# Optimization experiments

Measured on AMD Instinct MI355X. Metric: run time of the kernel, lower is better.

The kernel has to match this reference:

```python
import jax, jax.numpy as jnp
import numpy as np

B, S, H, D = 2, 2048, 16, 64  # batch, seq, heads, head_dim


def setup_inputs() -> dict:
    key = jax.random.key(0)
    kq, kk, kv = jax.random.split(key, 3)
    query = jax.random.normal(kq, (B, S, H, D), dtype=jnp.float32)
    key_l = jax.random.normal(kk, (B, S, H, D), dtype=jnp.float32)
    value = jax.random.normal(kv, (B, S, H, D), dtype=jnp.float32)
    # padding mask: all tokens valid
    attention_mask = jnp.ones((B, S), dtype=bool)
    # causal lower-triangular mask [1,1,S,S]
    causal_mask = jnp.tril(jnp.ones((S, S), dtype=bool))[None, None, :, :]
    return {"query": query, "key": key_l, "value": value,
            "attention_mask": attention_mask, "causal_mask": causal_mask}


def reference(query, key, value, attention_mask, causal_mask):
    b = query.shape[0]
    # broadcast causal mask to batch: (B,1,S,S)
    cm = jnp.broadcast_to(causal_mask, (b,) + causal_mask.shape[1:])
    # padding mask (B,S) -> (B,1,1,S), combine with causal
    am = attention_mask[:, None, None, :]
    mask = jnp.logical_and(cm, am)
    neg = jnp.finfo(query.dtype).min
    bias = jnp.where(mask, jnp.zeros((), query.dtype), jnp.full((), neg, query.dtype))
    sm_scale = 1.0 / jnp.sqrt(jnp.asarray(query.shape[-1], jnp.float32))
    # scores: (B,H,Sq,Sk)
    scores = jnp.einsum("bqhd,bkhd->bhqk", query, key) * sm_scale + bias
    # attention_softmax_in_fp32 = True
    probs = jax.nn.softmax(scores.astype(jnp.float32), axis=-1).astype(query.dtype)
    ctx = jnp.einsum("bhqk,bkhd->bqhd", probs, value)
    # merge heads -> hidden_size_per_partition
    return ctx.reshape(ctx.shape[0], ctx.shape[1], -1)
```

## Files before the change

### kernel.cpp

```cpp
#include <hip/hip_runtime.h>
#include <hip/hip_bf16.h>


typedef __attribute__((ext_vector_type(8))) short short8;
typedef __attribute__((ext_vector_type(4))) short short4v;
typedef __attribute__((ext_vector_type(4))) float f32x4;

__device__ __forceinline__ unsigned cvtpk(float a, float b) {
    __hip_bfloat162 h = __float22bfloat162_rn(make_float2(a, b));
    union { __hip_bfloat162 h; unsigned u; } c; c.h = h;
    return c.u;
}

__device__ __forceinline__ short8 pack8(float4 a, float4 b) {
    union { short8 s; unsigned u[4]; } w;
    w.u[0] = cvtpk(a.x, a.y); w.u[1] = cvtpk(a.z, a.w);
    w.u[2] = cvtpk(b.x, b.y); w.u[3] = cvtpk(b.z, b.w);
    return w.s;
}

__device__ __forceinline__ unsigned short f2b(float v) {
    union { __hip_bfloat16 h; unsigned short u; } c;
    c.h = __float2bfloat16(v);
    return c.u;
}

__device__ __forceinline__ float b2f(unsigned short u) {
    union { unsigned u; float f; } v; v.u = ((unsigned)u) << 16;
    return v.f;
}

#define TR64(dst, addr) \
    asm volatile("ds_read_b64_tr_b16 %0, %1" : "=v"(dst) : "v"(addr))

#define GLOAD_LDS16(g, l) \
    __builtin_amdgcn_global_load_lds((const __attribute__((address_space(1))) void*)(g), \
                                     (__attribute__((address_space(3))) void*)(l), 16, 0, 0)

__constant__ unsigned char JOBS[24][3] = {
    {15,0,16},{7,0,16},{14,0,15},{14,15,30},{13,14,28},{6,0,14},{12,13,26},{11,12,24},
    {15,16,32},{13,0,14},{12,0,13},{10,0,11},{10,11,22},{9,0,10},{11,0,12},{5,0,12},
    {0,0,2},{1,0,4},{2,0,6},{3,0,8},{8,0,9},{9,10,20},{8,9,18},{4,0,10}
};

__global__ __launch_bounds__(256, 4)
void CoreAttention_68710886801875_prepass(const float* __restrict__ K,
                                          const float* __restrict__ V,
                                          unsigned short* __restrict__ Kbf,
                                          unsigned short* __restrict__ Vbf)
{
    const int tile = blockIdx.x;
    const int bh = tile >> 5, kt = tile & 31;
    const size_t base = (size_t)(bh >> 4) * (2048 * 1024) + (size_t)(bh & 15) * 64;
    unsigned short* ktile = Kbf + (size_t)tile * 4096;
    unsigned short* vtile = Vbf + (size_t)tile * 4096;

#pragma unroll
    for (int it = 0; it < 2; ++it) {
        const int c = threadIdx.x + it * 256;
        {
            const int r  = c >> 3;
            const int c8 = (c & 7) ^ (r & 7);
            const float* src = K + base + (size_t)(kt * 64 + r) * 1024 + c8 * 8;
            *(short8*)(ktile + c * 8) = pack8(*(const float4*)src, *(const float4*)(src + 4));
        }
        {
            const int s = c >> 3, k_lo = (c >> 1) & 3, half = c & 1;
            const int k  = (s >> 2) * 4 + k_lo;
            const int c8 = (s & 3) * 2 + half;
            const float* src = V + base + (size_t)(kt * 64 + k) * 1024 + c8 * 8;
            *(short8*)(vtile + c * 8) = pack8(*(const float4*)src, *(const float4*)(src + 4));
        }
    }
}

template <int PRE>
__global__ __launch_bounds__(256, 3)
void CoreAttention_68710886801875_kernel(const float* __restrict__ Q,
                                         const float* __restrict__ K,
                                         const float* __restrict__ V,
                                         const unsigned short* __restrict__ Kbf,
                                         const unsigned short* __restrict__ Vbf,
                                         float* __restrict__ O,
                                         unsigned short* __restrict__ Opart,
                                         float* __restrict__ Lpart)
{
    constexpr int S = 2048, HD = 1024;
    constexpr float SCALE = 0.125f * 1.44269504088896340736f;

    __shared__ __align__(16) unsigned short ldsK[2][64 * 64];
    __shared__ __align__(16) unsigned short ldsV[2][64 * 64];
    __shared__ __align__(16) unsigned short ldsPT[4][2][64 * 16];

    const int tid = threadIdx.x;
    const int wid = tid >> 6, lane = tid & 63, g = lane >> 4, lm = lane & 15;

    const int bx     = blockIdx.x;
    const int r_     = bx >> 3;
    const int jobIdx = r_ >> 2;
    const int bh     = (bx & 7) * 4 + (r_ & 3);
    const int qt     = JOBS[jobIdx][0];
    const int t0     = JOBS[jobIdx][1];
    const int t1     = JOBS[jobIdx][2];
    const int b      = bh >> 4, h = bh & 15;
    const int q0     = qt << 7;
    const int diagT  = 2 * qt + (wid >> 1);
    const int nd     = (wid & 1) << 1;
    const size_t base = ((size_t)b * S) * HD + (size_t)h * 64;

    const int r0 = tid >> 3, c8 = tid & 7;
    const float* kp0 = K + base + (size_t)r0 * HD + c8 * 8;
    const float* vp0 = V + base + (size_t)r0 * HD + c8 * 8;
    float4 kst[4], vst[4];
    const unsigned short* kbfB = Kbf + (size_t)bh * 32 * 4096;
    const unsigned short* vbfB = Vbf + (size_t)bh * 32 * 4096;

    auto STAGE_ISSUE = [&](int kt2, int buf) {
        if constexpr (PRE) {
            const unsigned short* ks = kbfB + (size_t)kt2 * 4096 + tid * 8;
            const unsigned short* vs = vbfB + (size_t)kt2 * 4096 + tid * 8;
            GLOAD_LDS16(ks,        &ldsK[buf][tid * 8]);
            GLOAD_LDS16(ks + 2048, &ldsK[buf][tid * 8 + 2048]);
            GLOAD_LDS16(vs,        &ldsV[buf][tid * 8]);
            GLOAD_LDS16(vs + 2048, &ldsV[buf][tid * 8 + 2048]);
        } else {
            const float* kp = kp0 + (size_t)kt2 * 64 * HD;
            const float* vp = vp0 + (size_t)kt2 * 64 * HD;
            kst[0] = *(const float4*)kp;
            kst[1] = *(const float4*)(kp + 4);
            kst[2] = *(const float4*)(kp + (size_t)32 * HD);
            kst[3] = *(const float4*)(kp + (size_t)32 * HD + 4);
            vst[0] = *(const float4*)vp;
            vst[1] = *(const float4*)(vp + 4);
            vst[2] = *(const float4*)(vp + (size_t)32 * HD);
            vst[3] = *(const float4*)(vp + (size_t)32 * HD + 4);
        }
    };
    auto STAGE_WRITE = [&](int buf) {
        if constexpr (!PRE) {
#pragma unroll
            for (int it = 0; it < 2; ++it) {
                const int r = r0 + it * 32;
                const unsigned byteK = (unsigned)((r * 128 + c8 * 16) ^ ((r & 7) << 4));
                *(short8*)((char*)&ldsK[buf][0] + byteK) = pack8(kst[it * 2], kst[it * 2 + 1]);
                const unsigned byteV = (unsigned)(((r >> 2) * 4 + (c8 >> 1)) * 128 +
                                                  (r & 3) * 32 + (c8 & 1) * 16);
                *(short8*)((char*)&ldsV[buf][0] + byteV) = pack8(vst[it * 2], vst[it * 2 + 1]);
            }
        }
    };

    short8 qf[2][2];
#pragma unroll
    for (int m = 0; m < 2; ++m) {
        const float* qp = Q + base + (size_t)(q0 + wid * 32 + m * 16 + lm) * HD + g * 8;
#pragma unroll
        for (int ks = 0; ks < 2; ++ks) {
            float4 a = *(const float4*)(qp + ks * 32);
            float4 cc = *(const float4*)(qp + ks * 32 + 4);
            a.x *= SCALE; a.y *= SCALE; a.z *= SCALE; a.w *= SCALE;
            cc.x *= SCALE; cc.y *= SCALE; cc.z *= SCALE; cc.w *= SCALE;
            qf[m][ks] = pack8(a, cc);
        }
    }

    short8 ones;
#pragma unroll
    for (int j = 0; j < 8; ++j) ones[j] = (short)0x3F80;

    f32x4 oacc[2][4], lacc[2];
#pragma unroll
    for (int m = 0; m < 2; ++m) {
        lacc[m] = (f32x4){0.f, 0.f, 0.f, 0.f};
#pragma unroll
        for (int n = 0; n < 4; ++n) oacc[m][n] = (f32x4){0.f, 0.f, 0.f, 0.f};
    }

    const unsigned vBase = (unsigned)(size_t)&ldsV[0][0];
    const unsigned ptAddr = (unsigned)(size_t)&ldsPT[wid][0][0];

    STAGE_ISSUE(t0, 0);
    STAGE_WRITE(0);
    __syncthreads();

    for (int t = t0; t < t1; ++t) {
        const int cur = (t - t0) & 1;
        if (t + 1 < t1) STAGE_ISSUE(t + 1, cur ^ 1);

        if (t <= diagT) {
            const bool full = (t < diagT);

            f32x4 sv[2][4];
            __builtin_amdgcn_s_setprio(1);
#pragma unroll
            for (int n = 0; n < 4; ++n) {
                short8 kf0, kf1;
                if (full || n <= nd + 1) {
                    const int kr = n * 16 + lm;
                    const unsigned b0 = cur * 8192u +
                        (unsigned)((kr * 128 + g * 16) ^ ((kr & 7) << 4));
                    const unsigned b1 = cur * 8192u +
                        (unsigned)((kr * 128 + 64 + g * 16) ^ ((kr & 7) << 4));
                    kf0 = *(const short8*)((const char*)&ldsK[0][0] + b0);
                    kf1 = *(const short8*)((const char*)&ldsK[0][0] + b1);
                }
#pragma unroll
                for (int m = 0; m < 2; ++m) {
                    if (full || n <= nd + m) {
                        f32x4 acc = (f32x4){0.f, 0.f, 0.f, 0.f};
                        acc = __builtin_amdgcn_mfma_f32_16x16x32_bf16(qf[m][0], kf0, acc, 0, 0, 0);
                        acc = __builtin_amdgcn_mfma_f32_16x16x32_bf16(qf[m][1], kf1, acc, 0, 0, 0);
                        if (!full && n == nd + m) {
#pragma unroll
                            for (int r = 0; r < 4; ++r)
                                if (lm > g * 4 + r) acc[r] = -1e30f;
                        }
                        sv[m][n] = acc;
                    } else {
                        sv[m][n] = (f32x4){-1e30f, -1e30f, -1e30f, -1e30f};
                    }
                }
            }
            __builtin_amdgcn_s_setprio(0);

#pragma unroll
            for (int m = 0; m < 2; ++m)
#pragma unroll
                for (int n = 0; n < 4; ++n) {
                    float p[4];
#pragma unroll
                    for (int r = 0; r < 4; ++r) p[r] = exp2f(sv[m][n][r]);
                    union { short4v s; unsigned uu[2]; } pk;
                    pk.uu[0] = cvtpk(p[0], p[1]);
                    pk.uu[1] = cvtpk(p[2], p[3]);
                    const unsigned byte = (unsigned)((n * 4 + (lm >> 2)) * 128 +
                                                     (lm & 3) * 32 + g * 8);
                    *(short4v*)((char*)&ldsPT[wid][m][0] + byte) = pk.s;
                }

            asm volatile("s_waitcnt lgkmcnt(0)" ::: "memory");
            short4v vlo[2][4], vhi[2][4], pL[2][2], pH[2][2];
#pragma unroll
            for (int ks = 0; ks < 2; ++ks) {
                const unsigned sub = (unsigned)(8 * ks + 2 * g);
#pragma unroll
                for (int n = 0; n < 4; ++n) {
                    const unsigned va = vBase + cur * 8192u + (sub * 4 + n) * 128 + lm * 8;
                    TR64(vlo[ks][n], va);
                    TR64(vhi[ks][n], va + 512);
                }
#pragma unroll
                for (int m = 0; m < 2; ++m) {
                    const unsigned pa = ptAddr + m * 2048u + sub * 128 + lm * 8;
                    TR64(pL[m][ks], pa);
                    TR64(pH[m][ks], pa + 128);
                }
            }
            asm volatile("s_waitcnt lgkmcnt(0)" ::: "memory");
            __builtin_amdgcn_sched_barrier(0);
            __builtin_amdgcn_s_setprio(1);
#pragma unroll
            for (int m = 0; m < 2; ++m)
#pragma unroll
                for (int ks = 0; ks < 2; ++ks) {
                    const short8 pf = __builtin_shufflevector(pL[m][ks], pH[m][ks],
                                                              0, 1, 2, 3, 4, 5, 6, 7);
                    lacc[m] = __builtin_amdgcn_mfma_f32_16x16x32_bf16(pf, ones, lacc[m], 0, 0, 0);
#pragma unroll
                    for (int n = 0; n < 4; ++n) {
                        const short8 vf = __builtin_shufflevector(vlo[ks][n], vhi[ks][n],
                                                                  0, 1, 2, 3, 4, 5, 6, 7);
                        oacc[m][n] = __builtin_amdgcn_mfma_f32_16x16x32_bf16(pf, vf,
                                                                             oacc[m][n], 0, 0, 0);
                    }
                }
            __builtin_amdgcn_s_setprio(0);
        }

        if (t + 1 < t1) STAGE_WRITE(cur ^ 1);
        __syncthreads();
    }

    if (qt >= 8) {
        const int part = ((bh * 8 + (qt - 8)) << 1) + (t0 != 0 ? 1 : 0);
        unsigned short* op = Opart + (size_t)part * 8192;
        float* lp = Lpart + part * 128;
#pragma unroll
        for (int m = 0; m < 2; ++m)
#pragma unroll
            for (int r = 0; r < 4; ++r) {
                const int row = wid * 32 + m * 16 + g * 4 + r;
                if (lm == 0) lp[row] = lacc[m][r];
#pragma unroll
                for (int n = 0; n < 4; ++n)
                    op[row * 64 + n * 16 + lm] = f2b(oacc[m][n][r]);
            }
    } else {
#pragma unroll
        for (int m = 0; m < 2; ++m)
#pragma unroll
            for (int r = 0; r < 4; ++r) {
                const float inv = 1.0f / lacc[m][r];
                const int row = q0 + wid * 32 + m * 16 + g * 4 + r;
                float* op = O + base + (size_t)row * HD;
#pragma unroll
                for (int n = 0; n < 4; ++n)
                    op[n * 16 + lm] = oacc[m][n][r] * inv;
            }
    }
}

__global__ __launch_bounds__(256, 8)
void CoreAttention_68710886801875_combine(const unsigned short* __restrict__ Opart,
                                          const float* __restrict__ Lpart,
                                          float* __restrict__ O)
{
    const int sid = blockIdx.x;
    const int bh = sid >> 3, qt = 8 + (sid & 7);
    const size_t base = (size_t)(bh >> 4) * (2048 * 1024) + (size_t)(bh & 15) * 64;
    const unsigned short* A = Opart + (size_t)sid * 2 * 8192;
    const unsigned short* Bp = A + 8192;
    const float* la = Lpart + sid * 2 * 128;
    const float* lb = la + 128;

    const int tid = threadIdx.x;
    const int r = tid >> 1;
    const int c0 = (tid & 1) * 32;
    const float inv = 1.0f / (la[r] + lb[r]);
    float* op = O + base + (size_t)(qt * 128 + r) * 1024;
#pragma unroll
    for (int j = 0; j < 32; ++j) {
        const int c = c0 + j;
        op[c] = (b2f(A[r * 64 + c]) + b2f(Bp[r * 64 + c])) * inv;
    }
}

extern "C" void kernel_launch(void* const* d_in, const int* in_sizes, int n_in,
                              void* d_out, int out_size, void* d_ws, size_t ws_size,
                              hipStream_t stream) {
    (void)in_sizes; (void)n_in; (void)out_size;
    const float* Q = (const float*)d_in[0];
    const float* K = (const float*)d_in[1];
    const float* V = (const float*)d_in[2];
    float* O = (float*)d_out;

    const size_t IMG    = 16777216ull;
    const size_t PART_O = 512ull * 8192 * 2;
    const size_t PART_L = 512ull * 128 * 4;

    if (ws_size >= IMG + PART_O + PART_L) {
        unsigned short* Kbf = (unsigned short*)d_ws;
        unsigned short* Vbf = Kbf + 4194304;
        unsigned short* Opart = (unsigned short*)((char*)d_ws + IMG);
        float* Lpart = (float*)((char*)d_ws + IMG + PART_O);
        hipLaunchKernelGGL(CoreAttention_68710886801875_prepass,
                           dim3(1024), dim3(256), 0, stream, K, V, Kbf, Vbf);
        hipLaunchKernelGGL((CoreAttention_68710886801875_kernel<1>),
                           dim3(768), dim3(256), 0, stream, Q, K, V, Kbf, Vbf, O,
                           Opart, Lpart);
        hipLaunchKernelGGL(CoreAttention_68710886801875_combine,
                           dim3(256), dim3(256), 0, stream, Opart, Lpart, O);
    } else {
        unsigned short* Opart = (unsigned short*)d_ws;
        float* Lpart = (float*)((char*)d_ws + PART_O);
        hipLaunchKernelGGL((CoreAttention_68710886801875_kernel<0>),
                           dim3(768), dim3(256), 0, stream, Q, K, V,
                           (const unsigned short*)nullptr, (const unsigned short*)nullptr,
                           O, Opart, Lpart);
        hipLaunchKernelGGL(CoreAttention_68710886801875_combine,
                           dim3(256), dim3(256), 0, stream, Opart, Lpart, O);
    }
}
```

Baseline: 62.59 us.

## Rebalance causal split-K schedule into 30 jobs with three-way splits and smaller LDS

Replaces the 24-job split-KV schedule with a 30-job table that splits late query tiles into up to three KV partitions. The first partition writes unnormalized fp32 output straight to O, and the combine kernel reads it back alongside one or two bf16 partials. The P-tile LDS buffer is halved by processing one m at a time, and occupancy is raised to 4 blocks per CU. This is meant to even out per-block work and the wave tail across the 960-block grid. It costs more partial traffic, a read-modify-write of O in combine, and more serialized LDS waits per m iteration.

```diff
diff --git a/kernel.cpp b/kernel.cpp
--- a/kernel.cpp
+++ b/kernel.cpp
@@ -37,10 +37,15 @@
     __builtin_amdgcn_global_load_lds((const __attribute__((address_space(1))) void*)(g), \
                                      (__attribute__((address_space(3))) void*)(l), 16, 0, 0)
 
-__constant__ unsigned char JOBS[24][3] = {
-    {15,0,16},{7,0,16},{14,0,15},{14,15,30},{13,14,28},{6,0,14},{12,13,26},{11,12,24},
-    {15,16,32},{13,0,14},{12,0,13},{10,0,11},{10,11,22},{9,0,10},{11,0,12},{5,0,12},
-    {0,0,2},{1,0,4},{2,0,6},{3,0,8},{8,0,9},{9,10,20},{8,9,18},{4,0,10}
+__constant__ unsigned char JOBS[30][5] = {
+    {15, 0,11, 0,0},{14, 0,10, 0,0},{ 9, 0,10, 0,0},{13,10,19, 8,1},
+    {12, 9,18, 6,1},{13, 0,10, 0,0},{11, 0,12, 0,0},{10, 0,11, 0,0},
+    {15,11,22,12,1},{14,10,20,10,1},{ 9,10,20, 3,1},{13,19,28, 9,2},
+    { 8, 0, 9, 0,0},{12,18,26, 7,2},{11,12,24, 5,1},{10,11,22, 4,1},
+    {15,22,32,13,2},{14,20,30,11,2},{ 3, 0, 8, 0,0},{12, 0, 9, 0,0},
+    { 8, 9,18, 2,1},{ 7, 0, 8, 0,0},{ 5, 0,12, 0,0},{ 4, 0,10, 0,0},
+    { 0, 0, 2, 0,0},{ 1, 0, 4, 0,0},{ 2, 0, 6, 0,0},{ 6, 0, 7, 0,0},
+    { 6, 7,14, 0,1},{ 7, 8,16, 1,1}
 };
 
 __global__ __launch_bounds__(256, 4)
@@ -75,7 +80,7 @@
 }
 
 template <int PRE>
-__global__ __launch_bounds__(256, 3)
+__global__ __launch_bounds__(256, 4)
 void CoreAttention_68710886801875_kernel(const float* __restrict__ Q,
                                          const float* __restrict__ K,
                                          const float* __restrict__ V,
@@ -90,7 +95,7 @@
 
     __shared__ __align__(16) unsigned short ldsK[2][64 * 64];
     __shared__ __align__(16) unsigned short ldsV[2][64 * 64];
-    __shared__ __align__(16) unsigned short ldsPT[4][2][64 * 16];
+    __shared__ __align__(16) unsigned short ldsPT[4][64 * 16];
 
     const int tid = threadIdx.x;
     const int wid = tid >> 6, lane = tid & 63, g = lane >> 4, lm = lane & 15;
@@ -177,7 +182,7 @@
     }
 
     const unsigned vBase = (unsigned)(size_t)&ldsV[0][0];
-    const unsigned ptAddr = (unsigned)(size_t)&ldsPT[wid][0][0];
+    const unsigned ptAddr = (unsigned)(size_t)&ldsPT[wid][0];
 
     STAGE_ISSUE(t0, 0);
     STAGE_WRITE(0);
@@ -223,8 +228,20 @@
             }
             __builtin_amdgcn_s_setprio(0);
 
-#pragma unroll
-            for (int m = 0; m < 2; ++m)
+            short4v vlo[2][4], vhi[2][4];
+#pragma unroll
+            for (int ks = 0; ks < 2; ++ks) {
+                const unsigned sub = (unsigned)(8 * ks + 2 * g);
+#pragma unroll
+                for (int n = 0; n < 4; ++n) {
+                    const unsigned va = vBase + cur * 8192u + (sub * 4 + n) * 128 + lm * 8;
+                    TR64(vlo[ks][n], va);
+                    TR64(vhi[ks][n], va + 512);
+                }
+            }
+
+#pragma unroll
+            for (int m = 0; m < 2; ++m) {
 #pragma unroll
                 for (int n = 0; n < 4; ++n) {
                     float p[4];
@@ -235,35 +252,22 @@
                     pk.uu[1] = cvtpk(p[2], p[3]);
                     const unsigned byte = (unsigned)((n * 4 + (lm >> 2)) * 128 +
                                                      (lm & 3) * 32 + g * 8);
-                    *(short4v*)((char*)&ldsPT[wid][m][0] + byte) = pk.s;
-                }
-
-            asm volatile("s_waitcnt lgkmcnt(0)" ::: "memory");
-            short4v vlo[2][4], vhi[2][4], pL[2][2], pH[2][2];
-#pragma unroll
-            for (int ks = 0; ks < 2; ++ks) {
-                const unsigned sub = (unsigned)(8 * ks + 2 * g);
-#pragma unroll
-                for (int n = 0; n < 4; ++n) {
-                    const unsigned va = vBase + cur * 8192u + (sub * 4 + n) * 128 + lm * 8;
-                    TR64(vlo[ks][n], va);
-                    TR64(vhi[ks][n], va + 512);
-                }
-#pragma unroll
-                for (int m = 0; m < 2; ++m) {
-                    const unsigned pa = ptAddr + m * 2048u + sub * 128 + lm * 8;
-                    TR64(pL[m][ks], pa);
-                    TR64(pH[m][ks], pa + 128);
-                }
-            }
-            asm volatile("s_waitcnt lgkmcnt(0)" ::: "memory");
-            __builtin_amdgcn_sched_barrier(0);
-            __builtin_amdgcn_s_setprio(1);
-#pragma unroll
-            for (int m = 0; m < 2; ++m)
+                    *(short4v*)((char*)&ldsPT[wid][0] + byte) = pk.s;
+                }
+                asm volatile("s_waitcnt lgkmcnt(0)" ::: "memory");
+                short4v pL[2], pH[2];
 #pragma unroll
                 for (int ks = 0; ks < 2; ++ks) {
-                    const short8 pf = __builtin_shufflevector(pL[m][ks], pH[m][ks],
+                    const unsigned pa = ptAddr + (unsigned)(8 * ks + 2 * g) * 128 + lm * 8;
+                    TR64(pL[ks], pa);
+                    TR64(pH[ks], pa + 128);
+                }
+                asm volatile("s_waitcnt lgkmcnt(0)" ::: "memory");
+                __builtin_amdgcn_sched_barrier(0);
+                __builtin_amdgcn_s_setprio(1);
+#pragma unroll
+                for (int ks = 0; ks < 2; ++ks) {
+                    const short8 pf = __builtin_shufflevector(pL[ks], pH[ks],
                                                               0, 1, 2, 3, 4, 5, 6, 7);
                     lacc[m] = __builtin_amdgcn_mfma_f32_16x16x32_bf16(pf, ones, lacc[m], 0, 0, 0);
 #pragma unroll
@@ -274,28 +278,15 @@
                                                                              oacc[m][n], 0, 0, 0);
                     }
                 }
-            __builtin_amdgcn_s_setprio(0);
+                __builtin_amdgcn_s_setprio(0);
+            }
         }
 
         if (t + 1 < t1) STAGE_WRITE(cur ^ 1);
         __syncthreads();
     }
 
-    if (qt >= 8) {
-        const int part = ((bh * 8 + (qt - 8)) << 1) + (t0 != 0 ? 1 : 0);
-        unsigned short* op = Opart + (size_t)part * 8192;
-        float* lp = Lpart + part * 128;
-#pragma unroll
-        for (int m = 0; m < 2; ++m)
-#pragma unroll
-            for (int r = 0; r < 4; ++r) {
-                const int row = wid * 32 + m * 16 + g * 4 + r;
-                if (lm == 0) lp[row] = lacc[m][r];
-#pragma unroll
-                for (int n = 0; n < 4; ++n)
-                    op[row * 64 + n * 16 + lm] = f2b(oacc[m][n][r]);
-            }
-    } else {
+    if (qt <= 5) {
 #pragma unroll
         for (int m = 0; m < 2; ++m)
 #pragma unroll
@@ -306,6 +297,36 @@
 #pragma unroll
                 for (int n = 0; n < 4; ++n)
                     op[n * 16 + lm] = oacc[m][n][r] * inv;
+            }
+    } else if (t0 == 0) {
+        const int tile = bh * 10 + (qt - 6);
+        float* lp = Lpart + (size_t)tile * 3 * 128;
+#pragma unroll
+        for (int m = 0; m < 2; ++m)
+#pragma unroll
+            for (int r = 0; r < 4; ++r) {
+                const int row = wid * 32 + m * 16 + g * 4 + r;
+                if (lm == 0) lp[row] = lacc[m][r];
+                float* op = O + base + (size_t)(q0 + row) * HD;
+#pragma unroll
+                for (int n = 0; n < 4; ++n)
+                    op[n * 16 + lm] = oacc[m][n][r];
+            }
+    } else {
+        const int tile = bh * 10 + (qt - 6);
+        const int slot = JOBS[jobIdx][3];
+        const int p    = JOBS[jobIdx][4];
+        unsigned short* op = Opart + (size_t)(bh * 14 + slot) * 8192;
+        float* lp = Lpart + ((size_t)tile * 3 + p) * 128;
+#pragma unroll
+        for (int m = 0; m < 2; ++m)
+#pragma unroll
+            for (int r = 0; r < 4; ++r) {
+                const int row = wid * 32 + m * 16 + g * 4 + r;
+                if (lm == 0) lp[row] = lacc[m][r];
+#pragma unroll
+                for (int n = 0; n < 4; ++n)
+                    op[row * 64 + n * 16 + lm] = f2b(oacc[m][n][r]);
             }
     }
 }
@@ -316,22 +337,28 @@
                                           float* __restrict__ O)
 {
     const int sid = blockIdx.x;
-    const int bh = sid >> 3, qt = 8 + (sid & 7);
+    const int bh = sid / 10, tt = sid % 10;
+    const int qt = tt + 6;
+    const int np = (qt >= 12) ? 3 : 2;
     const size_t base = (size_t)(bh >> 4) * (2048 * 1024) + (size_t)(bh & 15) * 64;
-    const unsigned short* A = Opart + (size_t)sid * 2 * 8192;
-    const unsigned short* Bp = A + 8192;
-    const float* la = Lpart + sid * 2 * 128;
-    const float* lb = la + 128;
+    const int slot1 = (qt <= 11) ? tt : (6 + 2 * (qt - 12));
+    const unsigned short* P1 = Opart + (size_t)(bh * 14 + slot1) * 8192;
+    const unsigned short* P2 = P1 + 8192;
+    const float* lp = Lpart + (size_t)sid * 3 * 128;
 
     const int tid = threadIdx.x;
     const int r = tid >> 1;
     const int c0 = (tid & 1) * 32;
-    const float inv = 1.0f / (la[r] + lb[r]);
-    float* op = O + base + (size_t)(qt * 128 + r) * 1024;
+    float lsum = lp[r] + lp[128 + r];
+    if (np == 3) lsum += lp[256 + r];
+    const float inv = 1.0f / lsum;
+    float* op = O + base + (size_t)(qt * 128 + r) * 1024 + c0;
+    const int ro = r * 64 + c0;
 #pragma unroll
     for (int j = 0; j < 32; ++j) {
-        const int c = c0 + j;
-        op[c] = (b2f(A[r * 64 + c]) + b2f(Bp[r * 64 + c])) * inv;
+        float acc = op[j] + b2f(P1[ro + j]);
+        if (np == 3) acc += b2f(P2[ro + j]);
+        op[j] = acc * inv;
     }
 }
 
@@ -345,8 +372,8 @@
     float* O = (float*)d_out;
 
     const size_t IMG    = 16777216ull;
-    const size_t PART_O = 512ull * 8192 * 2;
-    const size_t PART_L = 512ull * 128 * 4;
+    const size_t PART_O = 448ull * 8192 * 2;
+    const size_t PART_L = 320ull * 3 * 128 * 4;
 
     if (ws_size >= IMG + PART_O + PART_L) {
         unsigned short* Kbf = (unsigned short*)d_ws;
@@ -356,18 +383,18 @@
         hipLaunchKernelGGL(CoreAttention_68710886801875_prepass,
                            dim3(1024), dim3(256), 0, stream, K, V, Kbf, Vbf);
         hipLaunchKernelGGL((CoreAttention_68710886801875_kernel<1>),
-                           dim3(768), dim3(256), 0, stream, Q, K, V, Kbf, Vbf, O,
+                           dim3(960), dim3(256), 0, stream, Q, K, V, Kbf, Vbf, O,
                            Opart, Lpart);
         hipLaunchKernelGGL(CoreAttention_68710886801875_combine,
-                           dim3(256), dim3(256), 0, stream, Opart, Lpart, O);
+                           dim3(320), dim3(256), 0, stream, Opart, Lpart, O);
     } else {
         unsigned short* Opart = (unsigned short*)d_ws;
         float* Lpart = (float*)((char*)d_ws + PART_O);
         hipLaunchKernelGGL((CoreAttention_68710886801875_kernel<0>),
-                           dim3(768), dim3(256), 0, stream, Q, K, V,
+                           dim3(960), dim3(256), 0, stream, Q, K, V,
                            (const unsigned short*)nullptr, (const unsigned short*)nullptr,
                            O, Opart, Lpart);
         hipLaunchKernelGGL(CoreAttention_68710886801875_combine,
-                           dim3(256), dim3(256), 0, stream, Opart, Lpart, O);
-    }
-}
+                           dim3(320), dim3(256), 0, stream, Opart, Lpart, O);
+    }
+}
```

Result: slower. 129.0 us (+106.1%).

## Rebalance causal attention work with finer split-K job table and 3-way combine

Applied to the files above, without the earlier changes.

Adds a new job table that splits long causal query tiles into two or three KV chunks, raising the grid from 768 to 960 blocks with more even per-block work. Partial outputs go to per-slot buffers, and the combine kernel merges two or three partials for query tiles 6-15. The aim is a shorter tail of the longest blocks on the GPU, in exchange for more partial writes and a larger combine pass. The old table stays as a fallback when workspace is small.

```diff
diff --git a/kernel.cpp b/kernel.cpp
--- a/kernel.cpp
+++ b/kernel.cpp
@@ -37,10 +37,24 @@
     __builtin_amdgcn_global_load_lds((const __attribute__((address_space(1))) void*)(g), \
                                      (__attribute__((address_space(3))) void*)(l), 16, 0, 0)
 
-__constant__ unsigned char JOBS[24][3] = {
-    {15,0,16},{7,0,16},{14,0,15},{14,15,30},{13,14,28},{6,0,14},{12,13,26},{11,12,24},
-    {15,16,32},{13,0,14},{12,0,13},{10,0,11},{10,11,22},{9,0,10},{11,0,12},{5,0,12},
-    {0,0,2},{1,0,4},{2,0,6},{3,0,8},{8,0,9},{9,10,20},{8,9,18},{4,0,10}
+__constant__ unsigned char JOBS_A[30][4] = {
+    {11,0,12,10},{11,12,24,11},{5,0,12,255},
+    {15,0,11,21},{15,11,22,22},{10,0,11,8},{10,11,22,9},
+    {15,22,32,23},{14,0,10,18},{14,10,20,19},{14,20,30,20},{13,0,10,15},
+    {9,0,10,6},{9,10,20,7},{4,0,10,255},
+    {13,10,19,16},{13,19,28,17},{12,0,9,12},{12,9,18,13},{8,0,9,4},{8,9,18,5},
+    {12,18,26,14},{7,0,8,2},{7,8,16,3},{3,0,8,255},
+    {6,0,7,0},{6,7,14,1},
+    {2,0,6,255},{1,0,4,255},{0,0,2,255}
+};
+
+__constant__ unsigned char JOBS_B[24][4] = {
+    {15,0,16,14},{7,0,16,255},{14,0,15,12},{14,15,30,13},
+    {13,14,28,11},{6,0,14,255},{12,13,26,9},{11,12,24,7},
+    {15,16,32,15},{13,0,14,10},{12,0,13,8},{10,0,11,4},
+    {10,11,22,5},{9,0,10,2},{11,0,12,6},{5,0,12,255},
+    {0,0,2,255},{1,0,4,255},{2,0,6,255},{3,0,8,255},
+    {8,0,9,0},{9,10,20,3},{8,9,18,1},{4,0,10,255}
 };
 
 __global__ __launch_bounds__(256, 4)
@@ -74,7 +88,7 @@
     }
 }
 
-template <int PRE>
+template <int PRE, int TBL>
 __global__ __launch_bounds__(256, 3)
 void CoreAttention_68710886801875_kernel(const float* __restrict__ Q,
                                          const float* __restrict__ K,
@@ -86,6 +100,7 @@
                                          float* __restrict__ Lpart)
 {
     constexpr int S = 2048, HD = 1024;
+    constexpr int NSLOT = TBL ? 16 : 24;
     constexpr float SCALE = 0.125f * 1.44269504088896340736f;
 
     __shared__ __align__(16) unsigned short ldsK[2][64 * 64];
@@ -95,17 +110,22 @@
     const int tid = threadIdx.x;
     const int wid = tid >> 6, lane = tid & 63, g = lane >> 4, lm = lane & 15;
 
-    const int bx     = blockIdx.x;
-    const int r_     = bx >> 3;
-    const int jobIdx = r_ >> 2;
-    const int bh     = (bx & 7) * 4 + (r_ & 3);
-    const int qt     = JOBS[jobIdx][0];
-    const int t0     = JOBS[jobIdx][1];
-    const int t1     = JOBS[jobIdx][2];
-    const int b      = bh >> 4, h = bh & 15;
-    const int q0     = qt << 7;
-    const int diagT  = 2 * qt + (wid >> 1);
-    const int nd     = (wid & 1) << 1;
+    int qt, t0, t1, slot, bh;
+    const int bx = blockIdx.x;
+    if constexpr (TBL == 0) {
+        const int j = bx >> 5;
+        bh = bx & 31;
+        qt = JOBS_A[j][0]; t0 = JOBS_A[j][1]; t1 = JOBS_A[j][2]; slot = JOBS_A[j][3];
+    } else {
+        const int r_ = bx >> 3;
+        const int j = r_ >> 2;
+        bh = (bx & 7) * 4 + (r_ & 3);
+        qt = JOBS_B[j][0]; t0 = JOBS_B[j][1]; t1 = JOBS_B[j][2]; slot = JOBS_B[j][3];
+    }
+    const int b  = bh >> 4, h = bh & 15;
+    const int q0 = qt << 7;
+    const int diagT = 2 * qt + (wid >> 1);
+    const int nd = (wid & 1) << 1;
     const size_t base = ((size_t)b * S) * HD + (size_t)h * 64;
 
     const int r0 = tid >> 3, c8 = tid & 7;
@@ -281,21 +301,7 @@
         __syncthreads();
     }
 
-    if (qt >= 8) {
-        const int part = ((bh * 8 + (qt - 8)) << 1) + (t0 != 0 ? 1 : 0);
-        unsigned short* op = Opart + (size_t)part * 8192;
-        float* lp = Lpart + part * 128;
-#pragma unroll
-        for (int m = 0; m < 2; ++m)
-#pragma unroll
-            for (int r = 0; r < 4; ++r) {
-                const int row = wid * 32 + m * 16 + g * 4 + r;
-                if (lm == 0) lp[row] = lacc[m][r];
-#pragma unroll
-                for (int n = 0; n < 4; ++n)
-                    op[row * 64 + n * 16 + lm] = f2b(oacc[m][n][r]);
-            }
-    } else {
+    if (slot == 255) {
 #pragma unroll
         for (int m = 0; m < 2; ++m)
 #pragma unroll
@@ -307,31 +313,53 @@
                 for (int n = 0; n < 4; ++n)
                     op[n * 16 + lm] = oacc[m][n][r] * inv;
             }
-    }
-}
-
+    } else {
+        unsigned short* op = Opart + (size_t)(bh * NSLOT + slot) * 8192;
+        float* lp = Lpart + (size_t)(bh * NSLOT + slot) * 128;
+#pragma unroll
+        for (int m = 0; m < 2; ++m)
+#pragma unroll
+            for (int r = 0; r < 4; ++r) {
+                const int row = wid * 32 + m * 16 + g * 4 + r;
+                if (lm == 0) lp[row] = lacc[m][r];
+#pragma unroll
+                for (int n = 0; n < 4; ++n)
+                    op[row * 64 + n * 16 + lm] = f2b(oacc[m][n][r]);
+            }
+    }
+}
+
+template <int TBL>
 __global__ __launch_bounds__(256, 8)
 void CoreAttention_68710886801875_combine(const unsigned short* __restrict__ Opart,
                                           const float* __restrict__ Lpart,
                                           float* __restrict__ O)
 {
+    constexpr int NSLOT = TBL ? 16 : 24;
+    constexpr int NT    = TBL ? 8 : 10;
     const int sid = blockIdx.x;
-    const int bh = sid >> 3, qt = 8 + (sid & 7);
+    const int bh = sid / NT, ti = sid % NT;
+    const int qt = ti + (TBL ? 8 : 6);
+    const int np = TBL ? 2 : ((qt >= 12) ? 3 : 2);
+    const int sb = TBL ? (qt - 8) * 2
+                       : ((qt < 12) ? (qt - 6) * 2 : 12 + (qt - 12) * 3);
     const size_t base = (size_t)(bh >> 4) * (2048 * 1024) + (size_t)(bh & 15) * 64;
-    const unsigned short* A = Opart + (size_t)sid * 2 * 8192;
-    const unsigned short* Bp = A + 8192;
-    const float* la = Lpart + sid * 2 * 128;
-    const float* lb = la + 128;
+    const unsigned short* P0 = Opart + (size_t)(bh * NSLOT + sb) * 8192;
+    const float* l0 = Lpart + (size_t)(bh * NSLOT + sb) * 128;
 
     const int tid = threadIdx.x;
     const int r = tid >> 1;
     const int c0 = (tid & 1) * 32;
-    const float inv = 1.0f / (la[r] + lb[r]);
-    float* op = O + base + (size_t)(qt * 128 + r) * 1024;
+    float lsum = l0[r] + l0[128 + r];
+    if (np == 3) lsum += l0[256 + r];
+    const float inv = 1.0f / lsum;
+    float* op = O + base + (size_t)(qt * 128 + r) * 1024 + c0;
+    const int ro = r * 64 + c0;
 #pragma unroll
     for (int j = 0; j < 32; ++j) {
-        const int c = c0 + j;
-        op[c] = (b2f(A[r * 64 + c]) + b2f(Bp[r * 64 + c])) * inv;
+        float acc = b2f(P0[ro + j]) + b2f(P0[8192 + ro + j]);
+        if (np == 3) acc += b2f(P0[16384 + ro + j]);
+        op[j] = acc * inv;
     }
 }
 
@@ -344,30 +372,53 @@
     const float* V = (const float*)d_in[2];
     float* O = (float*)d_out;
 
-    const size_t IMG    = 16777216ull;
-    const size_t PART_O = 512ull * 8192 * 2;
-    const size_t PART_L = 512ull * 128 * 4;
-
-    if (ws_size >= IMG + PART_O + PART_L) {
+    const size_t IMG = 16777216ull;
+    const size_t A_O = 32ull * 24 * 16384;
+    const size_t A_L = 32ull * 24 * 128 * 4;
+    const size_t B_O = 32ull * 16 * 16384;
+    const size_t B_L = 32ull * 16 * 128 * 4;
+
+    if (ws_size >= IMG + A_O + A_L) {
         unsigned short* Kbf = (unsigned short*)d_ws;
         unsigned short* Vbf = Kbf + 4194304;
         unsigned short* Opart = (unsigned short*)((char*)d_ws + IMG);
-        float* Lpart = (float*)((char*)d_ws + IMG + PART_O);
+        float* Lpart = (float*)((char*)d_ws + IMG + A_O);
         hipLaunchKernelGGL(CoreAttention_68710886801875_prepass,
                            dim3(1024), dim3(256), 0, stream, K, V, Kbf, Vbf);
-        hipLaunchKernelGGL((CoreAttention_68710886801875_kernel<1>),
+        hipLaunchKernelGGL((CoreAttention_68710886801875_kernel<1, 0>),
+                           dim3(960), dim3(256), 0, stream, Q, K, V, Kbf, Vbf, O,
+                           Opart, Lpart);
+        hipLaunchKernelGGL((CoreAttention_68710886801875_combine<0>),
+                           dim3(320), dim3(256), 0, stream, Opart, Lpart, O);
+    } else if (ws_size >= IMG + B_O + B_L) {
+        unsigned short* Kbf = (unsigned short*)d_ws;
+        unsigned short* Vbf = Kbf + 4194304;
+        unsigned short* Opart = (unsigned short*)((char*)d_ws + IMG);
+        float* Lpart = (float*)((char*)d_ws + IMG + B_O);
+        hipLaunchKernelGGL(CoreAttention_68710886801875_prepass,
+                           dim3(1024), dim3(256), 0, stream, K, V, Kbf, Vbf);
+        hipLaunchKernelGGL((CoreAttention_68710886801875_kernel<1, 1>),
                            dim3(768), dim3(256), 0, stream, Q, K, V, Kbf, Vbf, O,
                            Opart, Lpart);
-        hipLaunchKernelGGL(CoreAttention_68710886801875_combine,
+        hipLaunchKernelGGL((CoreAttention_68710886801875_combine<1>),
                            dim3(256), dim3(256), 0, stream, Opart, Lpart, O);
+    } else if (ws_size >= A_O + A_L) {
+        unsigned short* Opart = (unsigned short*)d_ws;
+        float* Lpart = (float*)((char*)d_ws + A_O);
+        hipLaunchKernelGGL((CoreAttention_68710886801875_kernel<0, 0>),
+                           dim3(960), dim3(256), 0, stream, Q, K, V,
+                           (const unsigned short*)nullptr, (const unsigned short*)nullptr,
+                           O, Opart, Lpart);
+        hipLaunchKernelGGL((CoreAttention_68710886801875_combine<0>),
+                           dim3(320), dim3(256), 0, stream, Opart, Lpart, O);
     } else {
         unsigned short* Opart = (unsigned short*)d_ws;
-        float* Lpart = (float*)((char*)d_ws + PART_O);
-        hipLaunchKernelGGL((CoreAttention_68710886801875_kernel<0>),
+        float* Lpart = (float*)((char*)d_ws + B_O);
+        hipLaunchKernelGGL((CoreAttention_68710886801875_kernel<0, 1>),
                            dim3(768), dim3(256), 0, stream, Q, K, V,
                            (const unsigned short*)nullptr, (const unsigned short*)nullptr,
                            O, Opart, Lpart);
-        hipLaunchKernelGGL(CoreAttention_68710886801875_combine,
+        hipLaunchKernelGGL((CoreAttention_68710886801875_combine<1>),
                            dim3(256), dim3(256), 0, stream, Opart, Lpart, O);
     }
 }
```

Result: slower. 94.68 us (+51.3%).

## Fuse split-K combine into attention kernel via atomic last-block reduction

Applied to the files above, without the earlier changes.

Removes the separate combine kernel. Each split partial block writes its bf16 partial output and row sums, fences, and bumps an atomic counter. The second block to finish reads the sibling partial and writes the normalized final output. This trades one kernel launch and a global round trip of both partials for a memset of the flags, a fence, an atomic, and a tail of work on the last block.

```diff
diff --git a/kernel.cpp b/kernel.cpp
--- a/kernel.cpp
+++ b/kernel.cpp
@@ -37,10 +37,13 @@
     __builtin_amdgcn_global_load_lds((const __attribute__((address_space(1))) void*)(g), \
                                      (__attribute__((address_space(3))) void*)(l), 16, 0, 0)
 
-__constant__ unsigned char JOBS[24][3] = {
-    {15,0,16},{7,0,16},{14,0,15},{14,15,30},{13,14,28},{6,0,14},{12,13,26},{11,12,24},
-    {15,16,32},{13,0,14},{12,0,13},{10,0,11},{10,11,22},{9,0,10},{11,0,12},{5,0,12},
-    {0,0,2},{1,0,4},{2,0,6},{3,0,8},{8,0,9},{9,10,20},{8,9,18},{4,0,10}
+__constant__ unsigned char JOBS[24][4] = {
+    {15,0,16,14},{7,0,16,255},{14,0,15,12},{14,15,30,13},
+    {13,14,28,11},{6,0,14,255},{12,13,26,9},{11,12,24,7},
+    {15,16,32,15},{13,0,14,10},{12,0,13,8},{10,0,11,4},
+    {10,11,22,5},{9,0,10,2},{11,0,12,6},{5,0,12,255},
+    {0,0,2,255},{1,0,4,255},{2,0,6,255},{3,0,8,255},
+    {8,0,9,0},{9,10,20,3},{8,9,18,1},{4,0,10,255}
 };
 
 __global__ __launch_bounds__(256, 4)
@@ -83,7 +86,8 @@
                                          const unsigned short* __restrict__ Vbf,
                                          float* __restrict__ O,
                                          unsigned short* __restrict__ Opart,
-                                         float* __restrict__ Lpart)
+                                         float* __restrict__ Lpart,
+                                         int* __restrict__ Flags)
 {
     constexpr int S = 2048, HD = 1024;
     constexpr float SCALE = 0.125f * 1.44269504088896340736f;
@@ -91,6 +95,7 @@
     __shared__ __align__(16) unsigned short ldsK[2][64 * 64];
     __shared__ __align__(16) unsigned short ldsV[2][64 * 64];
     __shared__ __align__(16) unsigned short ldsPT[4][2][64 * 16];
+    __shared__ int amLast;
 
     const int tid = threadIdx.x;
     const int wid = tid >> 6, lane = tid & 63, g = lane >> 4, lm = lane & 15;
@@ -102,6 +107,7 @@
     const int qt     = JOBS[jobIdx][0];
     const int t0     = JOBS[jobIdx][1];
     const int t1     = JOBS[jobIdx][2];
+    const int slot   = JOBS[jobIdx][3];
     const int b      = bh >> 4, h = bh & 15;
     const int q0     = qt << 7;
     const int diagT  = 2 * qt + (wid >> 1);
@@ -281,21 +287,7 @@
         __syncthreads();
     }
 
-    if (qt >= 8) {
-        const int part = ((bh * 8 + (qt - 8)) << 1) + (t0 != 0 ? 1 : 0);
-        unsigned short* op = Opart + (size_t)part * 8192;
-        float* lp = Lpart + part * 128;
-#pragma unroll
-        for (int m = 0; m < 2; ++m)
-#pragma unroll
-            for (int r = 0; r < 4; ++r) {
-                const int row = wid * 32 + m * 16 + g * 4 + r;
-                if (lm == 0) lp[row] = lacc[m][r];
-#pragma unroll
-                for (int n = 0; n < 4; ++n)
-                    op[row * 64 + n * 16 + lm] = f2b(oacc[m][n][r]);
-            }
-    } else {
+    if (slot == 255) {
 #pragma unroll
         for (int m = 0; m < 2; ++m)
 #pragma unroll
@@ -307,31 +299,41 @@
                 for (int n = 0; n < 4; ++n)
                     op[n * 16 + lm] = oacc[m][n][r] * inv;
             }
-    }
-}
-
-__global__ __launch_bounds__(256, 8)
-void CoreAttention_68710886801875_combine(const unsigned short* __restrict__ Opart,
-                                          const float* __restrict__ Lpart,
-                                          float* __restrict__ O)
-{
-    const int sid = blockIdx.x;
-    const int bh = sid >> 3, qt = 8 + (sid & 7);
-    const size_t base = (size_t)(bh >> 4) * (2048 * 1024) + (size_t)(bh & 15) * 64;
-    const unsigned short* A = Opart + (size_t)sid * 2 * 8192;
-    const unsigned short* Bp = A + 8192;
-    const float* la = Lpart + sid * 2 * 128;
-    const float* lb = la + 128;
-
-    const int tid = threadIdx.x;
-    const int r = tid >> 1;
-    const int c0 = (tid & 1) * 32;
-    const float inv = 1.0f / (la[r] + lb[r]);
-    float* op = O + base + (size_t)(qt * 128 + r) * 1024;
-#pragma unroll
-    for (int j = 0; j < 32; ++j) {
-        const int c = c0 + j;
-        op[c] = (b2f(A[r * 64 + c]) + b2f(Bp[r * 64 + c])) * inv;
+    } else {
+        unsigned short* op = Opart + (size_t)(bh * 16 + slot) * 8192;
+        float* lp = Lpart + (size_t)(bh * 16 + slot) * 128;
+#pragma unroll
+        for (int m = 0; m < 2; ++m)
+#pragma unroll
+            for (int r = 0; r < 4; ++r) {
+                const int row = wid * 32 + m * 16 + g * 4 + r;
+                if (lm == 0) lp[row] = lacc[m][r];
+#pragma unroll
+                for (int n = 0; n < 4; ++n)
+                    op[row * 64 + n * 16 + lm] = f2b(oacc[m][n][r]);
+            }
+        __threadfence();
+        __syncthreads();
+        if (tid == 0)
+            amLast = (atomicAdd(&Flags[bh * 8 + (qt - 8)], 1) == 1);
+        __syncthreads();
+        if (amLast) {
+            __threadfence();
+            const unsigned short* pop = Opart + (size_t)(bh * 16 + (slot ^ 1)) * 8192;
+            const float* plp = Lpart + (size_t)(bh * 16 + (slot ^ 1)) * 128;
+#pragma unroll
+            for (int m = 0; m < 2; ++m)
+#pragma unroll
+                for (int r = 0; r < 4; ++r) {
+                    const int row = wid * 32 + m * 16 + g * 4 + r;
+                    const float inv = 1.0f / (lacc[m][r] + plp[row]);
+                    float* o = O + base + (size_t)(q0 + row) * HD;
+#pragma unroll
+                    for (int n = 0; n < 4; ++n)
+                        o[n * 16 + lm] = (oacc[m][n][r] +
+                                          b2f(pop[row * 64 + n * 16 + lm])) * inv;
+                }
+        }
     }
 }
 
@@ -345,29 +347,30 @@
     float* O = (float*)d_out;
 
     const size_t IMG    = 16777216ull;
-    const size_t PART_O = 512ull * 8192 * 2;
+    const size_t PART_O = 512ull * 16384;
     const size_t PART_L = 512ull * 128 * 4;
-
-    if (ws_size >= IMG + PART_O + PART_L) {
+    const size_t FLAGS  = 1024ull;
+
+    if (ws_size >= IMG + PART_O + PART_L + FLAGS) {
         unsigned short* Kbf = (unsigned short*)d_ws;
         unsigned short* Vbf = Kbf + 4194304;
         unsigned short* Opart = (unsigned short*)((char*)d_ws + IMG);
         float* Lpart = (float*)((char*)d_ws + IMG + PART_O);
+        int* Flags = (int*)((char*)d_ws + IMG + PART_O + PART_L);
+        hipMemsetAsync(Flags, 0, FLAGS, stream);
         hipLaunchKernelGGL(CoreAttention_68710886801875_prepass,
                            dim3(1024), dim3(256), 0, stream, K, V, Kbf, Vbf);
         hipLaunchKernelGGL((CoreAttention_68710886801875_kernel<1>),
                            dim3(768), dim3(256), 0, stream, Q, K, V, Kbf, Vbf, O,
-                           Opart, Lpart);
-        hipLaunchKernelGGL(CoreAttention_68710886801875_combine,
-                           dim3(256), dim3(256), 0, stream, Opart, Lpart, O);
+                           Opart, Lpart, Flags);
     } else {
         unsigned short* Opart = (unsigned short*)d_ws;
         float* Lpart = (float*)((char*)d_ws + PART_O);
+        int* Flags = (int*)((char*)d_ws + PART_O + PART_L);
+        hipMemsetAsync(Flags, 0, FLAGS, stream);
         hipLaunchKernelGGL((CoreAttention_68710886801875_kernel<0>),
                            dim3(768), dim3(256), 0, stream, Q, K, V,
                            (const unsigned short*)nullptr, (const unsigned short*)nullptr,
-                           O, Opart, Lpart);
-        hipLaunchKernelGGL(CoreAttention_68710886801875_combine,
-                           dim3(256), dim3(256), 0, stream, Opart, Lpart, O);
-    }
-}
+                           O, Opart, Lpart, Flags);
+    }
+}
```

Result: slower. 157.1 us (+150.9%).
